# Optimization experiments

Measured on AMD Instinct MI355X. Metric: run time of the kernel, lower is better.

Reference implementation:

```python
import jax, jax.numpy as jnp
import numpy as np

COMMIT_LAMBDA = 0.25


def setup_inputs() -> dict:
    key = jax.random.key(0)
    k1, k2 = jax.random.split(key)
    B, C, T = 8, 256, 1024
    NCB, K, D = 2, 8192, 128
    x = jax.random.normal(k1, (B, C, T), dtype=jnp.float32)
    # EMA codebook weights buffer (init: randn * 0.1)
    codebooks = jax.random.normal(k2, (NCB, K, D), dtype=jnp.float32) * 0.1
    return {"x": x, "codebooks": codebooks}


def reference(x, codebooks):
    B, C, T = x.shape
    ncb, K, d = codebooks.shape
    # [B, C, T] -> [B*T, ncb, d]
    xs = x.reshape(B, ncb, d, T).transpose(0, 3, 1, 2).reshape(B * T, ncb, d)
    # squared euclidean distances (argmin-equivalent to cdist)
    x2 = jnp.sum(xs * xs, axis=-1)[..., None]            # [N, ncb, 1]
    c2 = jnp.sum(codebooks * codebooks, axis=-1)[None]    # [1, ncb, K]
    xc = jnp.einsum('bnd,nkd->bnk', xs, codebooks)        # [N, ncb, K]
    d2 = x2 - 2.0 * xc + c2
    idx = jnp.argmin(d2, axis=-1)                         # [N, ncb] int
    # gather nearest code vectors: [N, ncb, d]
    q = codebooks[jnp.arange(ncb)[None, :], idx]
    # straight-through estimator
    q_st = xs + jax.lax.stop_gradient(q - xs)
    # commitment loss (training mode): sum over codebooks of mse(x_i, q_i.detach())
    loss = COMMIT_LAMBDA * jnp.sum(
        jnp.mean((xs - jax.lax.stop_gradient(q)) ** 2, axis=(0, 2))
    )
    # reassemble to [B, C, T]
    quantized = q_st.reshape(B, T, ncb, d).transpose(0, 2, 3, 1).reshape(B, C, T)
    indices = idx.reshape(B, T, ncb).transpose(0, 2, 1)   # [B, ncb, T]
    return quantized, indices, loss
```

## Files before the change

### kernel.cpp

```cpp
#include <hip/hip_runtime.h>
#include <hip/hip_bf16.h>

#define BB   8
#define TT   1024
#define NCBN 2
#define DD   128
#define KK   8192
#define MM   8192

constexpr int OUT_IDX_OFF  = BB * 256 * TT;
constexpr int OUT_LOSS_OFF = OUT_IDX_OFF + BB * NCBN * TT;

#define THR   0.45f
#define QCAP  2048
#define SCAP  2048

typedef __attribute__((ext_vector_type(8))) short   short8;
typedef __attribute__((ext_vector_type(4))) float   float4v;

__device__ __forceinline__ unsigned short f2bf(float v) {
    unsigned u = __float_as_uint(v);
    return (unsigned short)((u + 0x7FFFu + ((u >> 16) & 1u)) >> 16);
}

__device__ __forceinline__ unsigned short f2bf_dn(float v) {
    unsigned u = __float_as_uint(v);
    unsigned short h = (unsigned short)(u >> 16);
    if ((u & 0x80000000u) && (u & 0xFFFFu)) ++h;
    return h;
}

__device__ __forceinline__ void gl_lds16(const void* g, void* l) {
    __builtin_amdgcn_global_load_lds(
        (const __attribute__((address_space(1))) unsigned int*)g,
        (__attribute__((address_space(3))) unsigned int*)l, 16, 0, 0);
}

__global__ __launch_bounds__(256)
void pack_kernel(const float* __restrict__ x, const float* __restrict__ cb,
                 unsigned short* __restrict__ xbf, unsigned short* __restrict__ cbf,
                 float* __restrict__ x2, float* __restrict__ c2,
                 unsigned long long* __restrict__ pmin, float* __restrict__ out) {
    __shared__ float Ld[DD][65];
    const int gb  = blockIdx.x;
    const int tid = threadIdx.x;

    if (gb < 256) {
        const int bxn = gb & 15, ty = gb >> 4;
        const int b = bxn >> 1, n = bxn & 1;
        const int t0 = ty * 64;

        const float* base = x + ((size_t)(b * 256 + n * 128)) * TT + t0;
        const int dro = tid >> 2, q4 = tid & 3;
#pragma unroll
        for (int half = 0; half < 2; ++half) {
            int d = dro + half * 64;
            const float* rp = base + (size_t)d * TT + q4 * 16;
#pragma unroll
            for (int j = 0; j < 4; ++j) {
                float4 v = *(const float4*)(rp + j * 4);
                int t = q4 * 16 + j * 4;
                Ld[d][t + 0] = v.x; Ld[d][t + 1] = v.y;
                Ld[d][t + 2] = v.z; Ld[d][t + 3] = v.w;
            }
        }
        __syncthreads();

        if (tid < 64) {
            float s = 0.f;
            for (int d = 0; d < DD; ++d) { float v = Ld[d][tid]; s = fmaf(v, v, s); }
            x2[(size_t)n * MM + b * TT + t0 + tid] = s;
            pmin[(size_t)n * MM + b * TT + t0 + tid] = 0xFFFFFFFFFFFFFFFFull;
        }

        unsigned short* orow0 = xbf + ((size_t)n * MM + b * TT + t0) * DD;
#pragma unroll
        for (int pp = 0; pp < 4; ++pp) {
            int u = tid + pp * 256;
            int tt = u >> 4, sg = u & 15;
            unsigned short tmp[8];
#pragma unroll
            for (int j = 0; j < 8; ++j) tmp[j] = f2bf(Ld[sg * 8 + j][tt]);
            uint4 pk;
            pk.x = (unsigned)tmp[0] | ((unsigned)tmp[1] << 16);
            pk.y = (unsigned)tmp[2] | ((unsigned)tmp[3] << 16);
            pk.z = (unsigned)tmp[4] | ((unsigned)tmp[5] << 16);
            pk.w = (unsigned)tmp[6] | ((unsigned)tmp[7] << 16);
            *(uint4*)(orow0 + (size_t)tt * DD + sg * 8) = pk;
        }
    } else {
        int g = (gb - 256) * 256 + tid;
        if (g == 0) out[OUT_LOSS_OFF] = 0.f;
        const float4* crow = (const float4*)(cb + (size_t)g * DD);
        unsigned short* orow = cbf + (size_t)g * DD;
        float s = 0.f;
#pragma unroll 4
        for (int i2 = 0; i2 < 16; ++i2) {
            float4 v0 = crow[2 * i2];
            float4 v1 = crow[2 * i2 + 1];
            s = fmaf(v0.x, v0.x, s); s = fmaf(v0.y, v0.y, s);
            s = fmaf(v0.z, v0.z, s); s = fmaf(v0.w, v0.w, s);
            s = fmaf(v1.x, v1.x, s); s = fmaf(v1.y, v1.y, s);
            s = fmaf(v1.z, v1.z, s); s = fmaf(v1.w, v1.w, s);
            uint4 pk;
            pk.x = (unsigned)f2bf(v0.x) | ((unsigned)f2bf(v0.y) << 16);
            pk.y = (unsigned)f2bf(v0.z) | ((unsigned)f2bf(v0.w) << 16);
            pk.z = (unsigned)f2bf(v1.x) | ((unsigned)f2bf(v1.y) << 16);
            pk.w = (unsigned)f2bf(v1.z) | ((unsigned)f2bf(v1.w) << 16);
            *(uint4*)(orow + i2 * 8) = pk;
        }
        c2[g] = s;
    }
}

__device__ void rescore_one(int n, int m, int k,
                            const float* __restrict__ x, const float* __restrict__ cb,
                            const float* __restrict__ x2, const float* __restrict__ c2,
                            unsigned long long* __restrict__ pmin) {
    int b = m >> 10, t = m & (TT - 1);
    const float* xp = x + ((size_t)(b * 256 + n * 128)) * TT + t;
    const float* cp = cb + ((size_t)(n * KK + k)) * DD;
    float xc = 0.f;
    for (int d = 0; d < DD; ++d)
        xc = fmaf(xp[(size_t)d * TT], cp[d], xc);
    float u = x2[n * MM + m] - 2.0f * xc;
    float s = u + c2[n * KK + k];
    unsigned long long pk = ((unsigned long long)__float_as_uint(s) << 32) | (unsigned)k;
    atomicMin(pmin + (size_t)n * MM + m, pk);
}

__global__ __launch_bounds__(512, 4)
void screen_kernel(const unsigned short* __restrict__ xbf,
                   const unsigned short* __restrict__ cbf,
                   const float* __restrict__ c2,
                   const float* __restrict__ x,
                   const float* __restrict__ cb32,
                   const float* __restrict__ x2,
                   unsigned long long* __restrict__ pmin,
                   unsigned long long* __restrict__ spill) {
    __shared__ __align__(16) unsigned short Csh[2][128 * 128];
    __shared__ float          c2s[2][128];
    __shared__ unsigned int   minU[128];
    __shared__ unsigned int   qcnt;
    __shared__ unsigned int   queue[QCAP];
    __shared__ unsigned short queueY[QCAP];

    const int tid = threadIdx.x;
    const int id  = blockIdx.x;
    const int n   = id & 1;
    const int ks  = (id >> 1) & 3;
    const int qt  = id >> 3;
    const int m0  = qt * 128;
    const int k0  = ks * 2048;

    const int wave = tid >> 6, lane = tid & 63;
    const int cw = wave & 1, qw = wave >> 1;
    const int quad = lane >> 4, l15 = lane & 15;

    unsigned long long* spillp = spill + (size_t)id * SCAP;

    int goff[4];
#pragma unroll
    for (int p = 0; p < 4; ++p) {
        int u   = (p * 8 + wave) * 64 + lane;
        int row = u >> 4;
        int seg = (u & 15) ^ (row & 15);
        goff[p] = (row * DD + seg * 8) * 2;
    }

    const char*  asrc0 = (const char*)(cbf + ((size_t)n * KK + k0) * DD);
    const float* c2p   = c2 + (size_t)n * KK + k0;

    {
        const char* qsrc = (const char*)(xbf + ((size_t)n * MM + m0) * DD);
#pragma unroll
        for (int p = 0; p < 4; ++p)
            gl_lds16(qsrc + goff[p], &Csh[0][(p * 8 + wave) * 512]);
#pragma unroll
        for (int p = 0; p < 4; ++p)
            gl_lds16(asrc0 + goff[p], &Csh[1][(p * 8 + wave) * 512]);
    }
    if (tid < 32)  *(float4*)&c2s[1][tid * 4] = *(const float4*)(c2p + tid * 4);
    if (tid < 128) minU[tid] = 0xFFFFFFFFu;
    if (tid == 0)  qcnt = 0;
    __syncthreads();

    short8 bfr[2][4];
#pragma unroll
    for (int tq = 0; tq < 2; ++tq) {
        int q = qw * 32 + tq * 16 + l15;
#pragma unroll
        for (int k4 = 0; k4 < 4; ++k4) {
            int seg = k4 * 4 + quad;
            bfr[tq][k4] = *(const short8*)(&Csh[0][q * 128 + ((seg ^ l15) * 8)]);
        }
    }
    __syncthreads();

    float thr[2] = {3.4e38f, 3.4e38f};

    for (int it = 0; it <= 16; ++it) {
        const int sb   = it & 1;
        const int cbuf = sb ^ 1;
        const int dcur = (it < 16) ? it : 0;

        if (it < 16) {
            const int dn = (it + 1 < 16) ? (it + 1) : 0;
            const char* src = asrc0 + (size_t)dn * (128 * DD * 2);
#pragma unroll
            for (int p = 0; p < 4; ++p)
                gl_lds16(src + goff[p], &Csh[sb][(p * 8 + wave) * 512]);
            if (tid < 32)
                *(float4*)&c2s[sb][tid * 4] =
                    *(const float4*)(c2p + dn * 128 + tid * 4);
        }

        float4v acc[4][2];
#pragma unroll
        for (int tc = 0; tc < 4; ++tc)
#pragma unroll
            for (int tq = 0; tq < 2; ++tq)
                acc[tc][tq] = (float4v){0.f, 0.f, 0.f, 0.f};

#pragma unroll
        for (int k4 = 0; k4 < 4; ++k4) {
            short8 a[4];
#pragma unroll
            for (int tc = 0; tc < 4; ++tc) {
                int r = cw * 64 + tc * 16 + l15;
                int seg = k4 * 4 + quad;
                a[tc] = *(const short8*)(&Csh[cbuf][r * 128 + ((seg ^ l15) * 8)]);
            }
#pragma unroll
            for (int tc = 0; tc < 4; ++tc)
#pragma unroll
                for (int tq = 0; tq < 2; ++tq)
                    acc[tc][tq] = __builtin_amdgcn_mfma_f32_16x16x32_bf16(
                        a[tc], bfr[tq][k4], acc[tc][tq], 0, 0, 0);
        }

        float cmin[2] = {3.4e38f, 3.4e38f};
#pragma unroll
        for (int tc = 0; tc < 4; ++tc) {
            float4v c2r = *(const float4v*)(&c2s[cbuf][cw * 64 + tc * 16 + quad * 4]);
#pragma unroll
            for (int tq = 0; tq < 2; ++tq) {
                float y0 = fmaf(-2.0f, acc[tc][tq][0], c2r[0]);
                float y1 = fmaf(-2.0f, acc[tc][tq][1], c2r[1]);
                float y2 = fmaf(-2.0f, acc[tc][tq][2], c2r[2]);
                float y3 = fmaf(-2.0f, acc[tc][tq][3], c2r[3]);
                acc[tc][tq] = (float4v){y0, y1, y2, y3};
                cmin[tq] = fminf(cmin[tq],
                                 fminf(fminf(y0, y1), fminf(y2, y3)));
            }
        }
#pragma unroll
        for (int tq = 0; tq < 2; ++tq) {
            float v = cmin[tq];
            v = fminf(v, __shfl_xor(v, 16, 64));
            v = fminf(v, __shfl_xor(v, 32, 64));
            cmin[tq] = v;
        }

        if (it > 0) {
            float te[2];
#pragma unroll
            for (int tq = 0; tq < 2; ++tq)
                te[tq] = fminf(thr[tq], cmin[tq] + THR);
#pragma unroll
            for (int tc = 0; tc < 4; ++tc) {
#pragma unroll
                for (int tq = 0; tq < 2; ++tq) {
                    float4v yv = acc[tc][tq];
                    float m4 = fminf(fminf(yv[0], yv[1]), fminf(yv[2], yv[3]));
                    if (m4 <= te[tq]) {
#pragma unroll
                        for (int rg = 0; rg < 4; ++rg) {
                            if (yv[rg] <= te[tq]) {
                                unsigned idx  = atomicAdd(&qcnt, 1u);
                                unsigned code = (unsigned)(dcur * 128 + cw * 64 + tc * 16 + quad * 4 + rg);
                                unsigned q    = (unsigned)(qw * 32 + tq * 16 + l15);
                                unsigned ent  = (q << 11) | code;
                                if (idx < QCAP) {
                                    queue[idx]  = ent;
                                    queueY[idx] = f2bf_dn(yv[rg]);
                                } else if (idx < QCAP + SCAP) {
                                    spillp[idx - QCAP] =
                                        ((unsigned long long)ent << 32) |
                                        (unsigned long long)f2bf_dn(yv[rg]);
                                } else {
                                    rescore_one(n, m0 + (int)q, k0 + (int)code,
                                                x, cb32, x2, c2, pmin);
                                }
                            }
                        }
                    }
                }
            }
        }

        if (it < 16) {
#pragma unroll
            for (int tq = 0; tq < 2; ++tq) {
                if (quad == 0) {
                    unsigned u  = __float_as_uint(cmin[tq]);
                    unsigned mu = (u & 0x80000000u) ? ~u : (u | 0x80000000u);
                    atomicMin(&minU[qw * 32 + tq * 16 + l15], mu);
                }
            }
        }
        __syncthreads();
        if (it < 16) {
#pragma unroll
            for (int tq = 0; tq < 2; ++tq) {
                unsigned mu = minU[qw * 32 + tq * 16 + l15];
                unsigned u  = (mu & 0x80000000u) ? (mu & 0x7FFFFFFFu) : ~mu;
                thr[tq] = __uint_as_float(u) + THR;
            }
        }
    }

    unsigned total = qcnt;
    if (total > (unsigned)(QCAP + SCAP)) total = QCAP + SCAP;
    for (unsigned i = tid; i < total; i += 512) {
        unsigned ent; unsigned short y16;
        if (i < QCAP) { ent = queue[i]; y16 = queueY[i]; }
        else {
            unsigned long long se = spillp[i - QCAP];
            ent = (unsigned)(se >> 32); y16 = (unsigned short)se;
        }
        unsigned q   = ent >> 11;
        unsigned mu  = minU[q];
        unsigned u   = (mu & 0x80000000u) ? (mu & 0x7FFFFFFFu) : ~mu;
        float thrF   = __uint_as_float(u) + THR;
        float yv     = __uint_as_float((unsigned)y16 << 16);
        if (yv <= thrF)
            rescore_one(n, m0 + (int)q, k0 + (int)(ent & 2047u),
                        x, cb32, x2, c2, pmin);
    }
}

__global__ __launch_bounds__(256)
void gather_kernel(const float* __restrict__ x, const float* __restrict__ cb,
                   const unsigned long long* __restrict__ pmin,
                   float* __restrict__ out) {
    __shared__ float Cr[64][DD + 1];
    __shared__ int   kid[64];
    const int b = blockIdx.x >> 1, n = blockIdx.x & 1;
    const int t0 = blockIdx.y * 64;
    const int tid = threadIdx.x;

    if (tid < 64) {
        int t = t0 + tid;
        int k = (int)(pmin[(size_t)n * MM + b * TT + t] & 0xFFFFFFFFull);
        kid[tid] = k;
        out[OUT_IDX_OFF + (b * NCBN + n) * TT + t] = (float)k;
    }
    __syncthreads();

    {
        int row = tid >> 2, q4 = tid & 3;
        const float* cp = cb + ((size_t)n * KK + kid[row]) * DD + q4 * 32;
#pragma unroll
        for (int j = 0; j < 8; ++j) {
            float4 v = *(const float4*)(cp + j * 4);
            int d = q4 * 32 + j * 4;
            Cr[row][d + 0] = v.x; Cr[row][d + 1] = v.y;
            Cr[row][d + 2] = v.z; Cr[row][d + 3] = v.w;
        }
    }
    __syncthreads();

    float lsum = 0.f;
    const float* xb = x  + ((size_t)(b * 256 + n * 128)) * TT + t0;
    float*       ob = out + ((size_t)(b * 256 + n * 128)) * TT + t0;
#pragma unroll
    for (int pp = 0; pp < 8; ++pp) {
        int u  = tid + pp * 256;
        int d  = u >> 4, ts = (u & 15) * 4;
        float4 xv = *(const float4*)(xb + (size_t)d * TT + ts);
        float4 qv = { Cr[ts + 0][d], Cr[ts + 1][d], Cr[ts + 2][d], Cr[ts + 3][d] };
        *(float4*)(ob + (size_t)d * TT + ts) = qv;
        float e;
        e = xv.x - qv.x; lsum = fmaf(e, e, lsum);
        e = xv.y - qv.y; lsum = fmaf(e, e, lsum);
        e = xv.z - qv.z; lsum = fmaf(e, e, lsum);
        e = xv.w - qv.w; lsum = fmaf(e, e, lsum);
    }

#pragma unroll
    for (int o = 32; o > 0; o >>= 1) lsum += __shfl_down(lsum, o, 64);
    __shared__ float wsum[4];
    int lane = tid & 63, w = tid >> 6;
    if (lane == 0) wsum[w] = lsum;
    __syncthreads();
    if (tid == 0) {
        float tot = wsum[0] + wsum[1] + wsum[2] + wsum[3];
        atomicAdd(out + OUT_LOSS_OFF, tot * 2.384185791015625e-7f);
    }
}

extern "C" void kernel_launch(void* const* d_in, const int* in_sizes, int n_in,
                              void* d_out, int out_size, void* d_ws, size_t ws_size,
                              hipStream_t stream) {
    (void)in_sizes; (void)n_in; (void)out_size; (void)ws_size;
    const float* x  = (const float*)d_in[0];
    const float* cb = (const float*)d_in[1];
    float* out = (float*)d_out;

    char* ws = (char*)d_ws;
    unsigned short* xbf = (unsigned short*)(ws);
    unsigned short* cbf = (unsigned short*)(ws + (4u << 20));
    float* x2 = (float*)(ws + (8u << 20));
    float* c2 = (float*)(ws + (8u << 20) + (64u << 10));
    unsigned long long* pmin =
        (unsigned long long*)(ws + (8u << 20) + (128u << 10));

    unsigned long long* spill = (unsigned long long*)out;

    pack_kernel<<<dim3(320), 256, 0, stream>>>(x, cb, xbf, cbf, x2, c2, pmin, out);
    screen_kernel<<<dim3(512), 512, 0, stream>>>(xbf, cbf, c2, x, cb, x2, pmin,
                                                 spill);
    gather_kernel<<<dim3(16, 16), 256, 0, stream>>>(x, cb, pmin, out);
}
```

Baseline: 182.2 us.

## Derive loss from stored min distance and halve pack/gather tile size

After: 183.3 us (median of 2 runs). No clear change (+0.6%).

```diff
diff --git a/kernel.cpp b/kernel.cpp
--- a/kernel.cpp
+++ b/kernel.cpp
@@ -41,32 +41,28 @@
                  unsigned short* __restrict__ xbf, unsigned short* __restrict__ cbf,
                  float* __restrict__ x2, float* __restrict__ c2,
                  unsigned long long* __restrict__ pmin, float* __restrict__ out) {
-    __shared__ float Ld[DD][65];
+    __shared__ float Ld[DD][33];
     const int gb  = blockIdx.x;
     const int tid = threadIdx.x;
 
-    if (gb < 256) {
+    if (gb < 512) {
         const int bxn = gb & 15, ty = gb >> 4;
         const int b = bxn >> 1, n = bxn & 1;
-        const int t0 = ty * 64;
+        const int t0 = ty * 32;
 
         const float* base = x + ((size_t)(b * 256 + n * 128)) * TT + t0;
-        const int dro = tid >> 2, q4 = tid & 3;
-#pragma unroll
-        for (int half = 0; half < 2; ++half) {
-            int d = dro + half * 64;
-            const float* rp = base + (size_t)d * TT + q4 * 16;
-#pragma unroll
-            for (int j = 0; j < 4; ++j) {
-                float4 v = *(const float4*)(rp + j * 4);
-                int t = q4 * 16 + j * 4;
-                Ld[d][t + 0] = v.x; Ld[d][t + 1] = v.y;
-                Ld[d][t + 2] = v.z; Ld[d][t + 3] = v.w;
-            }
+#pragma unroll
+        for (int pp = 0; pp < 4; ++pp) {
+            int u = tid + pp * 256;
+            int d = u >> 3, sg = u & 7;
+            float4 v = *(const float4*)(base + (size_t)d * TT + sg * 4);
+            int t = sg * 4;
+            Ld[d][t + 0] = v.x; Ld[d][t + 1] = v.y;
+            Ld[d][t + 2] = v.z; Ld[d][t + 3] = v.w;
         }
         __syncthreads();
 
-        if (tid < 64) {
+        if (tid < 32) {
             float s = 0.f;
             for (int d = 0; d < DD; ++d) { float v = Ld[d][tid]; s = fmaf(v, v, s); }
             x2[(size_t)n * MM + b * TT + t0 + tid] = s;
@@ -75,7 +71,7 @@
 
         unsigned short* orow0 = xbf + ((size_t)n * MM + b * TT + t0) * DD;
 #pragma unroll
-        for (int pp = 0; pp < 4; ++pp) {
+        for (int pp = 0; pp < 2; ++pp) {
             int u = tid + pp * 256;
             int tt = u >> 4, sg = u & 15;
             unsigned short tmp[8];
@@ -89,7 +85,7 @@
             *(uint4*)(orow0 + (size_t)tt * DD + sg * 8) = pk;
         }
     } else {
-        int g = (gb - 256) * 256 + tid;
+        int g = (gb - 512) * 256 + tid;
         if (g == 0) out[OUT_LOSS_OFF] = 0.f;
         const float4* crow = (const float4*)(cb + (size_t)g * DD);
         unsigned short* orow = cbf + (size_t)g * DD;
@@ -341,62 +337,53 @@
 }
 
 __global__ __launch_bounds__(256)
-void gather_kernel(const float* __restrict__ x, const float* __restrict__ cb,
+void gather_kernel(const float* __restrict__ cb,
                    const unsigned long long* __restrict__ pmin,
                    float* __restrict__ out) {
-    __shared__ float Cr[64][DD + 1];
-    __shared__ int   kid[64];
+    __shared__ float Cr[32][DD + 1];
+    __shared__ int   kid[32];
     const int b = blockIdx.x >> 1, n = blockIdx.x & 1;
-    const int t0 = blockIdx.y * 64;
+    const int t0 = blockIdx.y * 32;
     const int tid = threadIdx.x;
 
-    if (tid < 64) {
+    float spart = 0.f;
+    if (tid < 32) {
         int t = t0 + tid;
-        int k = (int)(pmin[(size_t)n * MM + b * TT + t] & 0xFFFFFFFFull);
+        unsigned long long pk = pmin[(size_t)n * MM + b * TT + t];
+        int k = (int)(pk & 0xFFFFFFFFull);
         kid[tid] = k;
         out[OUT_IDX_OFF + (b * NCBN + n) * TT + t] = (float)k;
+        spart = __uint_as_float((unsigned)(pk >> 32));
     }
     __syncthreads();
 
     {
-        int row = tid >> 2, q4 = tid & 3;
-        const float* cp = cb + ((size_t)n * KK + kid[row]) * DD + q4 * 32;
-#pragma unroll
-        for (int j = 0; j < 8; ++j) {
+        int row = tid >> 3, q8 = tid & 7;
+        const float* cp = cb + ((size_t)n * KK + kid[row]) * DD + q8 * 16;
+#pragma unroll
+        for (int j = 0; j < 4; ++j) {
             float4 v = *(const float4*)(cp + j * 4);
-            int d = q4 * 32 + j * 4;
+            int d = q8 * 16 + j * 4;
             Cr[row][d + 0] = v.x; Cr[row][d + 1] = v.y;
             Cr[row][d + 2] = v.z; Cr[row][d + 3] = v.w;
         }
     }
     __syncthreads();
 
-    float lsum = 0.f;
-    const float* xb = x  + ((size_t)(b * 256 + n * 128)) * TT + t0;
-    float*       ob = out + ((size_t)(b * 256 + n * 128)) * TT + t0;
-#pragma unroll
-    for (int pp = 0; pp < 8; ++pp) {
+    float* ob = out + ((size_t)(b * 256 + n * 128)) * TT + t0;
+#pragma unroll
+    for (int pp = 0; pp < 4; ++pp) {
         int u  = tid + pp * 256;
-        int d  = u >> 4, ts = (u & 15) * 4;
-        float4 xv = *(const float4*)(xb + (size_t)d * TT + ts);
+        int d  = u >> 3, ts = (u & 7) * 4;
         float4 qv = { Cr[ts + 0][d], Cr[ts + 1][d], Cr[ts + 2][d], Cr[ts + 3][d] };
         *(float4*)(ob + (size_t)d * TT + ts) = qv;
-        float e;
-        e = xv.x - qv.x; lsum = fmaf(e, e, lsum);
-        e = xv.y - qv.y; lsum = fmaf(e, e, lsum);
-        e = xv.z - qv.z; lsum = fmaf(e, e, lsum);
-        e = xv.w - qv.w; lsum = fmaf(e, e, lsum);
-    }
-
-#pragma unroll
-    for (int o = 32; o > 0; o >>= 1) lsum += __shfl_down(lsum, o, 64);
-    __shared__ float wsum[4];
-    int lane = tid & 63, w = tid >> 6;
-    if (lane == 0) wsum[w] = lsum;
-    __syncthreads();
-    if (tid == 0) {
-        float tot = wsum[0] + wsum[1] + wsum[2] + wsum[3];
-        atomicAdd(out + OUT_LOSS_OFF, tot * 2.384185791015625e-7f);
+    }
+
+    if (tid < 32) {
+#pragma unroll
+        for (int o = 16; o > 0; o >>= 1) spart += __shfl_down(spart, o, 64);
+        if (tid == 0)
+            atomicAdd(out + OUT_LOSS_OFF, spart * 2.384185791015625e-7f);
     }
 }
 
@@ -418,8 +405,8 @@
 
     unsigned long long* spill = (unsigned long long*)out;
 
-    pack_kernel<<<dim3(320), 256, 0, stream>>>(x, cb, xbf, cbf, x2, c2, pmin, out);
+    pack_kernel<<<dim3(576), 256, 0, stream>>>(x, cb, xbf, cbf, x2, c2, pmin, out);
     screen_kernel<<<dim3(512), 512, 0, stream>>>(xbf, cbf, c2, x, cb, x2, pmin,
                                                  spill);
-    gather_kernel<<<dim3(16, 16), 256, 0, stream>>>(x, cb, pmin, out);
-}
+    gather_kernel<<<dim3(16, 32), 256, 0, stream>>>(cb, pmin, out);
+}
```
